# Kernel optimization log

Hardware: AMD Instinct MI355X
Metric: run time of the kernel (lower is better)

The kernel has to match this reference:

```python
import jax, jax.numpy as jnp
import numpy as np


def _make_area_table():
    # Surrogate for create_table_neighbour_code_to_surface_area((1,1,1)):
    # a fixed 256-entry lookup that is exactly 0 for the all-empty (0) and
    # all-full (255) neighbour codes and strictly positive otherwise, which
    # preserves the structure the loss relies on (gt_surface = area > 0,
    # gt_foreground = code==255, gt_background = code==0).
    pop = np.array([bin(c).count("1") for c in range(256)], dtype=np.float32)
    return (0.5 * np.minimum(pop, 8.0 - pop)).astype(np.float32)


def _conv3d(x, w):
    # x: [B,1,D,H,W], w: [1,1,2,2,2], VALID 2x2x2 sliding window
    return jax.lax.conv_general_dilated(
        x, w, window_strides=(1, 1, 1), padding="VALID",
        dimension_numbers=("NCDHW", "OIDHW", "NCDHW"))


def setup_inputs() -> dict:
    key = jax.random.key(0)
    k1, k2 = jax.random.split(key)
    B, D, H, W = 2, 128, 256, 256
    preds = jax.random.normal(k1, (B, 1, D, H, W), dtype=jnp.float32)
    targets = jax.random.randint(k2, (B, 1, D, H, W), 0, 2).astype(jnp.float32)
    power = (2.0 ** jnp.arange(8, dtype=jnp.float32)).reshape(1, 1, 2, 2, 2)
    kernel = jnp.ones((1, 1, 2, 2, 2), dtype=jnp.float32)
    area = jnp.asarray(_make_area_table())
    return {"preds": preds, "targets": targets, "power": power,
            "kernel": kernel, "area": area}


def reference(preds, targets, power, kernel, area):
    eps = 1e-5
    bsz = preds.shape[0]

    # log-prob that all 8 voxels of each 2x2x2 cube are foreground / background
    fg = jnp.exp(_conv3d(jax.nn.log_sigmoid(preds), kernel)).reshape(bsz, -1)
    bg = jnp.exp(_conv3d(jax.nn.log_sigmoid(-preds), kernel)).reshape(bsz, -1)
    surf = 1.0 - fg - bg

    # neighbour codes from binary targets (no grad path)
    codes = jax.lax.stop_gradient(_conv3d(targets, power)).astype(jnp.int32).reshape(bsz, -1)
    gt_area = area[codes.reshape(-1)].reshape(bsz, -1)
    gt_fg = (codes == 255).astype(jnp.float32)
    gt_bg = (codes == 0).astype(jnp.float32)
    gt_surf = (gt_area > 0).astype(jnp.float32)

    fg_dice = (2.0 * jnp.sum(fg * gt_fg, -1) + eps) / (jnp.sum(fg, -1) + jnp.sum(gt_fg, -1) + eps)
    bg_dice = (2.0 * jnp.sum(bg * gt_bg, -1) + eps) / (jnp.sum(bg, -1) + jnp.sum(gt_bg, -1) + eps)
    surf_dice = (2.0 * jnp.sum(surf * gt_area, -1) + eps) / (jnp.sum((surf + gt_surf) * gt_area, -1) + eps)

    dice = (fg_dice + bg_dice + surf_dice) / 3.0
    return 1.0 - jnp.mean(dice)
```

## Files before the change

### kernel.cpp

```cpp
#include <hip/hip_runtime.h>

typedef float f2 __attribute__((ext_vector_type(2)));

#define DD 128
#define HH 256
#define WW 256
#define OD 127
#define SLICE_F (HH*WW)
#define NBIN 64
#define CHUNK 8
#define ROWS_B 9216
#define STAGE_B 18432
#define NBUF 2

#define VMCNT0() asm volatile("s_waitcnt vmcnt(0)" ::: "memory")

struct Sl { f2 uu2[4]; f2 vv2[4]; f2 ps[4]; };

__device__ __forceinline__ void stage_slice(const float* __restrict__ pB,
                                            const float* __restrict__ tB,
                                            int slice, char* lb,
                                            int h0, int wv, int lane)
{
    #pragma unroll
    for (int i = 0; i < 5; ++i) {
        if (i == 4 && wv >= 2) break;
        const int L = i * 4 + wv;
        const int T = (L >= 9) ? 1 : 0;
        const int r = L - T * 9;
        const int grow = min(h0 + r, HH - 1);
        const float* g = (T ? tB : pB)
                       + ((size_t)slice << 16) + (grow << 8) + (lane << 2);
        void* l = lb + T * ROWS_B + r * 1024 + lane * 16;
        __builtin_amdgcn_global_load_lds(
            (const __attribute__((address_space(1))) void*)g,
            (__attribute__((address_space(3))) void*)l, 16, 0, 0);
    }
}

__device__ __forceinline__ void make_sl_lds(const char* buf, int wv, int lane, Sl& S)
{
    const float* sp = (const float*)buf;
    const float* st = (const float*)(buf + ROWS_B);
    const int ro = ((wv << 1) << 8) + (lane << 2);
    const float4 p0 = *(const float4*)(sp + ro);
    const float4 p1 = *(const float4*)(sp + ro + 256);
    const float4 p2 = *(const float4*)(sp + ro + 512);
    const float4 t0 = *(const float4*)(st + ro);
    const float4 t1 = *(const float4*)(st + ro + 256);
    const float4 t2 = *(const float4*)(st + ro + 512);

    float u0x=__expf(p0.x), u0y=__expf(p0.y), u0z=__expf(p0.z), u0w=__expf(p0.w);
    float u1x=__expf(p1.x), u1y=__expf(p1.y), u1z=__expf(p1.z), u1w=__expf(p1.w);
    float u2x=__expf(p2.x), u2y=__expf(p2.y), u2z=__expf(p2.z), u2w=__expf(p2.w);

    f2 uA0 = {u0x,u1x}, uB0 = {u1x,u2x};
    f2 uA1 = {u0y,u1y}, uB1 = {u1y,u2y};
    f2 uA2 = {u0z,u1z}, uB2 = {u1z,u2z};
    f2 uA3 = {u0w,u1w}, uB3 = {u1w,u2w};

    f2 W0 = uA0*uB0, W1 = uA1*uB1, W2 = uA2*uB2, W3 = uA3*uB3;
    f2 Q0 = (uA0+1.f)*(uB0+1.f);
    f2 Q1 = (uA1+1.f)*(uB1+1.f);
    f2 Q2 = (uA2+1.f)*(uB2+1.f);
    f2 Q3 = (uA3+1.f)*(uB3+1.f);
    f2 W4, Q4;
    W4.x = __shfl_down(W0.x, 1); W4.y = __shfl_down(W0.y, 1);
    Q4.x = __shfl_down(Q0.x, 1); Q4.y = __shfl_down(Q0.y, 1);

    S.uu2[0]=W0*W1; S.uu2[1]=W1*W2; S.uu2[2]=W2*W3; S.uu2[3]=W3*W4;
    S.vv2[0]=Q0*Q1; S.vv2[1]=Q1*Q2; S.vv2[2]=Q2*Q3; S.vv2[3]=Q3*Q4;

    f2 cs0 = {t0.x+t1.x, t1.x+t2.x};
    f2 cs1 = {t0.y+t1.y, t1.y+t2.y};
    f2 cs2 = {t0.z+t1.z, t1.z+t2.z};
    f2 cs3 = {t0.w+t1.w, t1.w+t2.w};
    f2 cs4; cs4.x = __shfl_down(cs0.x, 1); cs4.y = __shfl_down(cs0.y, 1);
    S.ps[0]=cs0+cs1; S.ps[1]=cs1+cs2; S.ps[2]=cs2+cs3; S.ps[3]=cs3+cs4;
}

__device__ __forceinline__ void do_cubes(const Sl& P, const Sl& C,
        const f2 vAll, const f2 v3,
        f2& aFG, f2& aF255, f2& aBG, f2& aBG0, f2& aSFA,
        f2& c255, f2& c0, f2& cMN)
{
    #pragma unroll
    for (int j = 0; j < 4; ++j) {
        f2 E = P.uu2[j] * C.uu2[j];
        f2 Q = P.vv2[j] * C.vv2[j];
        f2 vj = (j == 3) ? v3 : vAll;
        f2 r; r.x = __builtin_amdgcn_rcpf(Q.x); r.y = __builtin_amdgcn_rcpf(Q.y);
        r *= vj;
        f2 fg = E * r;
        f2 pop = P.ps[j] + C.ps[j];
        f2 i255, i0, mn;
        i255.x = fmaxf(pop.x - 7.f, 0.f); i255.y = fmaxf(pop.y - 7.f, 0.f);
        i0.x   = fmaxf(1.f - pop.x, 0.f); i0.y   = fmaxf(1.f - pop.y, 0.f);
        mn.x   = 4.f - fabsf(pop.x - 4.f); mn.y = 4.f - fabsf(pop.y - 4.f);
        mn *= vj;
        aFG  += fg;
        aBG  += r;
        aF255 = fg * i255 + aF255;
        aBG0  = r  * i0   + aBG0;
        c255  = i255 * vj + c255;
        c0    = i0   * vj + c0;
        aSFA  = (fg + r) * mn + aSFA;
        cMN  += mn;
    }
}

#define LAYER(SRC, DST, STAGE_OFF, READ_OFF)                                   \
    do {                                                                       \
        VMCNT0();                                                              \
        __builtin_amdgcn_s_barrier();                                          \
        __builtin_amdgcn_sched_barrier(0);                                     \
        if (t + 2 <= NT)                                                       \
            stage_slice(pB, tB, d0 + t + 2, smem + (STAGE_OFF), h0, wv, lane); \
        make_sl_lds(smem + (READ_OFF), wv, lane, DST);                         \
        do_cubes(SRC, DST, vAll, v3, aFG, aF255, aBG, aBG0, aSFA, c255, c0, cMN); \
    } while (0)

__global__ __launch_bounds__(256, 4)
void loss_main(const float* __restrict__ preds,
               const float* __restrict__ targets,
               float* __restrict__ ws)
{
    __shared__ __align__(16) char smem[NBUF * STAGE_B];

    const int lane = threadIdx.x & 63;
    const int wv   = threadIdx.x >> 6;

    const int nid = ((blockIdx.x & 7) << 7) + (blockIdx.x >> 3);
    const int x = nid & 31;
    const int y = (nid >> 5) & 15;
    const int b = nid >> 9;

    const int h0 = x << 3;
    const int d0 = y << 3;
    const int NT = min(CHUNK, OD - d0);

    const float* pB = preds   + (size_t)b * DD * SLICE_F;
    const float* tB = targets + (size_t)b * DD * SLICE_F;

    const int   myrow = h0 + (wv << 1);
    const float rv1 = (myrow + 1 < HH - 1) ? 1.f : 0.f;
    const float v63 = (lane == 63) ? 0.f : 1.f;
    const f2 vAll = {1.f, rv1};
    const f2 v3   = {v63, v63 * rv1};

    f2 aFG={0,0}, aF255={0,0}, aBG={0,0}, aBG0={0,0}, aSFA={0,0};
    f2 c255={0,0}, c0={0,0}, cMN={0,0};

    stage_slice(pB, tB, d0,     smem,           h0, wv, lane);
    stage_slice(pB, tB, d0 + 1, smem + STAGE_B, h0, wv, lane);
    VMCNT0();
    __builtin_amdgcn_s_barrier();
    __builtin_amdgcn_sched_barrier(0);

    Sl A, B;
    make_sl_lds(smem, wv, lane, A);

    int t = 0;
    for (;;) {
        LAYER(A, B, 0, STAGE_B);
        if (++t >= NT) break;
        LAYER(B, A, STAGE_B, 0);
        if (++t >= NT) break;
    }

    float acc[8] = {aFG.x+aFG.y, aF255.x+aF255.y, c255.x+c255.y,
                    aBG.x+aBG.y, aBG0.x+aBG0.y,   c0.x+c0.y,
                    aSFA.x+aSFA.y, cMN.x+cMN.y};
    #pragma unroll
    for (int i = 0; i < 8; ++i) {
        float v = acc[i];
        #pragma unroll
        for (int off = 32; off > 0; off >>= 1) v += __shfl_xor(v, off);
        acc[i] = v;
    }
    float mine = acc[0];
    mine = (lane == 1) ? acc[1] : mine;
    mine = (lane == 2) ? acc[2] : mine;
    mine = (lane == 3) ? acc[3] : mine;
    mine = (lane == 4) ? acc[4] : mine;
    mine = (lane == 5) ? acc[5] : mine;
    mine = (lane == 6) ? acc[6] : mine;
    mine = (lane == 7) ? acc[7] : mine;
    if (lane < 8) {
        int bin = nid & (NBIN - 1);
        atomicAdd(&ws[(bin * 2 + b) * 8 + lane], mine);
    }
}

__global__ void loss_final(const float* __restrict__ ws, float* __restrict__ out)
{
    __shared__ float s[16];
    const int t = threadIdx.x;
    if (t < 16) {
        float v = 0.f;
        #pragma unroll 4
        for (int x = 0; x < NBIN; ++x) v += ws[x * 16 + t];
        s[t] = v;
    }
    __syncthreads();
    if (t == 0) {
        const float eps = 1e-5f;
        float dice = 0.f;
        #pragma unroll
        for (int b = 0; b < 2; ++b) {
            const float* q = s + b * 8;
            float fg_dice = (2.f*q[1] + eps) / (q[0] + q[2] + eps);
            float bg_dice = (2.f*q[4] + eps) / (q[3] + q[5] + eps);
            float q6 = 0.5f * q[6];
            float q7 = 0.5f * q[7];
            float ss = q7 - q6;
            float sf_dice = (2.f*ss + eps) / (ss + q7 + eps);
            dice += fg_dice + bg_dice + sf_dice;
        }
        out[0] = 1.f - dice * (1.f/6.f);
    }
}

extern "C" void kernel_launch(void* const* d_in, const int* in_sizes, int n_in,
                              void* d_out, int out_size, void* d_ws, size_t ws_size,
                              hipStream_t stream)
{
    const float* preds   = (const float*)d_in[0];
    const float* targets = (const float*)d_in[1];
    float* ws = (float*)d_ws;

    hipMemsetAsync(ws, 0, NBIN * 16 * sizeof(float), stream);

    loss_main<<<1024, 256, 0, stream>>>(preds, targets, ws);
    loss_final<<<1, 64, 0, stream>>>(ws, (float*)d_out);
}
```

Baseline: 40.77 us.

## Pack binary targets into bitmasks in a pre-pass and halve depth chunk

Adds a pre-pass kernel that packs the float targets into 1-bit masks (bit 29 of the float encoding separates 0.0 from 1.0). The main kernel then stages these compact bits into LDS and builds the neighbour-code popcounts with __popc, instead of staging and summing full float target rows. The depth chunk per block is halved, the grid doubled, and the launch-bounds occupancy hint raised from 4 to 8, since the smaller LDS footprint allows more resident blocks. In exchange it adds an extra kernel launch and a full read of targets in the pre-pass, and halving the chunk raises how often slices are reloaded at chunk boundaries.

```diff
diff --git a/kernel.cpp b/kernel.cpp
--- a/kernel.cpp
+++ b/kernel.cpp
@@ -8,47 +8,71 @@
 #define OD 127
 #define SLICE_F (HH*WW)
 #define NBIN 64
-#define CHUNK 8
-#define ROWS_B 9216
-#define STAGE_B 18432
+#define CHUNK 4
+#define PRED_B 9216
+#define BITS_B 512
+#define STAGE_B (PRED_B + BITS_B)
 #define NBUF 2
+#define WS_BITS_OFF 4096
 
 #define VMCNT0() asm volatile("s_waitcnt vmcnt(0)" ::: "memory")
 
 struct Sl { f2 uu2[4]; f2 vv2[4]; f2 ps[4]; };
 
+__global__ __launch_bounds__(256)
+void pack_bits(const float* __restrict__ t, unsigned int* __restrict__ bits)
+{
+    const int tid = blockIdx.x * 256 + threadIdx.x;
+    const float4* p = (const float4*)(t + ((size_t)tid << 5));
+    unsigned int acc = 0;
+    #pragma unroll
+    for (int i = 0; i < 8; ++i) {
+        float4 v = p[i];
+        unsigned int n = ((__float_as_uint(v.x) >> 29) & 1u)
+                       | (((__float_as_uint(v.y) >> 29) & 1u) << 1)
+                       | (((__float_as_uint(v.z) >> 29) & 1u) << 2)
+                       | (((__float_as_uint(v.w) >> 29) & 1u) << 3);
+        acc |= n << (i * 4);
+    }
+    bits[tid] = acc;
+}
+
 __device__ __forceinline__ void stage_slice(const float* __restrict__ pB,
-                                            const float* __restrict__ tB,
+                                            const unsigned int* __restrict__ bB,
                                             int slice, char* lb,
                                             int h0, int wv, int lane)
 {
     #pragma unroll
-    for (int i = 0; i < 5; ++i) {
-        if (i == 4 && wv >= 2) break;
-        const int L = i * 4 + wv;
-        const int T = (L >= 9) ? 1 : 0;
-        const int r = L - T * 9;
-        const int grow = min(h0 + r, HH - 1);
-        const float* g = (T ? tB : pB)
-                       + ((size_t)slice << 16) + (grow << 8) + (lane << 2);
-        void* l = lb + T * ROWS_B + r * 1024 + lane * 16;
-        __builtin_amdgcn_global_load_lds(
-            (const __attribute__((address_space(1))) void*)g,
-            (__attribute__((address_space(3))) void*)l, 16, 0, 0);
+    for (int i = 0; i < 3; ++i) {
+        const int slot = i * 4 + wv;
+        if (slot < 9) {
+            const int grow = min(h0 + slot, HH - 1);
+            const float* g = pB + ((size_t)slice << 16) + (grow << 8) + (lane << 2);
+            void* l = lb + slot * 1024 + lane * 16;
+            __builtin_amdgcn_global_load_lds(
+                (const __attribute__((address_space(1))) void*)g,
+                (__attribute__((address_space(3))) void*)l, 16, 0, 0);
+        } else if (slot < 11) {
+            const int half = slot - 9;
+            const int row  = (half << 3) + (lane >> 3);
+            const int grow = min(h0 + row, HH - 1);
+            const unsigned int* g = bB + (((size_t)slice * HH + grow) << 3) + (lane & 7);
+            void* l = lb + PRED_B + half * 256 + lane * 4;
+            __builtin_amdgcn_global_load_lds(
+                (const __attribute__((address_space(1))) void*)g,
+                (__attribute__((address_space(3))) void*)l, 4, 0, 0);
+        }
     }
 }
 
 __device__ __forceinline__ void make_sl_lds(const char* buf, int wv, int lane, Sl& S)
 {
     const float* sp = (const float*)buf;
-    const float* st = (const float*)(buf + ROWS_B);
+    const unsigned int* bl = (const unsigned int*)(buf + PRED_B);
     const int ro = ((wv << 1) << 8) + (lane << 2);
     const float4 p0 = *(const float4*)(sp + ro);
     const float4 p1 = *(const float4*)(sp + ro + 256);
     const float4 p2 = *(const float4*)(sp + ro + 512);
-    const float4 t0 = *(const float4*)(st + ro);
-    const float4 t1 = *(const float4*)(st + ro + 256);
-    const float4 t2 = *(const float4*)(st + ro + 512);
 
     float u0x=__expf(p0.x), u0y=__expf(p0.y), u0z=__expf(p0.z), u0w=__expf(p0.w);
     float u1x=__expf(p1.x), u1y=__expf(p1.y), u1z=__expf(p1.z), u1w=__expf(p1.w);
@@ -71,12 +95,22 @@
     S.uu2[0]=W0*W1; S.uu2[1]=W1*W2; S.uu2[2]=W2*W3; S.uu2[3]=W3*W4;
     S.vv2[0]=Q0*Q1; S.vv2[1]=Q1*Q2; S.vv2[2]=Q2*Q3; S.vv2[3]=Q3*Q4;
 
-    f2 cs0 = {t0.x+t1.x, t1.x+t2.x};
-    f2 cs1 = {t0.y+t1.y, t1.y+t2.y};
-    f2 cs2 = {t0.z+t1.z, t1.z+t2.z};
-    f2 cs3 = {t0.w+t1.w, t1.w+t2.w};
-    f2 cs4; cs4.x = __shfl_down(cs0.x, 1); cs4.y = __shfl_down(cs0.y, 1);
-    S.ps[0]=cs0+cs1; S.ps[1]=cs1+cs2; S.ps[2]=cs2+cs3; S.ps[3]=cs3+cs4;
+    const int r = wv << 1;
+    const int q = lane >> 3;
+    const int sh = (lane & 7) << 2;
+    unsigned int a0 = bl[r*8 + q],     a1 = bl[r*8 + q + 1];
+    unsigned int b0 = bl[(r+1)*8 + q], b1 = bl[(r+1)*8 + q + 1];
+    unsigned int c0 = bl[(r+2)*8 + q], c1 = bl[(r+2)*8 + q + 1];
+    unsigned int m0 = (unsigned int)(((((unsigned long long)a1) << 32) | a0) >> sh) & 0x1Fu;
+    unsigned int m1 = (unsigned int)(((((unsigned long long)b1) << 32) | b0) >> sh) & 0x1Fu;
+    unsigned int m2 = (unsigned int)(((((unsigned long long)c1) << 32) | c0) >> sh) & 0x1Fu;
+    unsigned int M01 = m0 | (m1 << 8);
+    unsigned int M12 = m1 | (m2 << 8);
+    #pragma unroll
+    for (int j = 0; j < 4; ++j) {
+        S.ps[j].x = (float)__popc((M01 >> j) & 0x303u);
+        S.ps[j].y = (float)__popc((M12 >> j) & 0x303u);
+    }
 }
 
 __device__ __forceinline__ void do_cubes(const Sl& P, const Sl& C,
@@ -115,14 +149,14 @@
         __builtin_amdgcn_s_barrier();                                          \
         __builtin_amdgcn_sched_barrier(0);                                     \
         if (t + 2 <= NT)                                                       \
-            stage_slice(pB, tB, d0 + t + 2, smem + (STAGE_OFF), h0, wv, lane); \
+            stage_slice(pB, bB, d0 + t + 2, smem + (STAGE_OFF), h0, wv, lane); \
         make_sl_lds(smem + (READ_OFF), wv, lane, DST);                         \
         do_cubes(SRC, DST, vAll, v3, aFG, aF255, aBG, aBG0, aSFA, c255, c0, cMN); \
     } while (0)
 
-__global__ __launch_bounds__(256, 4)
+__global__ __launch_bounds__(256, 8)
 void loss_main(const float* __restrict__ preds,
-               const float* __restrict__ targets,
+               const unsigned int* __restrict__ bits,
                float* __restrict__ ws)
 {
     __shared__ __align__(16) char smem[NBUF * STAGE_B];
@@ -130,17 +164,17 @@
     const int lane = threadIdx.x & 63;
     const int wv   = threadIdx.x >> 6;
 
-    const int nid = ((blockIdx.x & 7) << 7) + (blockIdx.x >> 3);
+    const int nid = ((blockIdx.x & 7) << 8) + (blockIdx.x >> 3);
     const int x = nid & 31;
-    const int y = (nid >> 5) & 15;
-    const int b = nid >> 9;
+    const int y = (nid >> 5) & 31;
+    const int b = nid >> 10;
 
     const int h0 = x << 3;
-    const int d0 = y << 3;
+    const int d0 = y << 2;
     const int NT = min(CHUNK, OD - d0);
 
-    const float* pB = preds   + (size_t)b * DD * SLICE_F;
-    const float* tB = targets + (size_t)b * DD * SLICE_F;
+    const float*        pB = preds + (size_t)b * DD * SLICE_F;
+    const unsigned int* bB = bits  + (size_t)b * DD * HH * 8;
 
     const int   myrow = h0 + (wv << 1);
     const float rv1 = (myrow + 1 < HH - 1) ? 1.f : 0.f;
@@ -151,8 +185,8 @@
     f2 aFG={0,0}, aF255={0,0}, aBG={0,0}, aBG0={0,0}, aSFA={0,0};
     f2 c255={0,0}, c0={0,0}, cMN={0,0};
 
-    stage_slice(pB, tB, d0,     smem,           h0, wv, lane);
-    stage_slice(pB, tB, d0 + 1, smem + STAGE_B, h0, wv, lane);
+    stage_slice(pB, bB, d0,     smem,           h0, wv, lane);
+    stage_slice(pB, bB, d0 + 1, smem + STAGE_B, h0, wv, lane);
     VMCNT0();
     __builtin_amdgcn_s_barrier();
     __builtin_amdgcn_sched_barrier(0);
@@ -228,9 +262,11 @@
     const float* preds   = (const float*)d_in[0];
     const float* targets = (const float*)d_in[1];
     float* ws = (float*)d_ws;
+    unsigned int* bitsbuf = (unsigned int*)((char*)d_ws + WS_BITS_OFF);
 
     hipMemsetAsync(ws, 0, NBIN * 16 * sizeof(float), stream);
 
-    loss_main<<<1024, 256, 0, stream>>>(preds, targets, ws);
+    pack_bits<<<2048, 256, 0, stream>>>(targets, bitsbuf);
+    loss_main<<<2048, 256, 0, stream>>>(preds, bitsbuf, ws);
     loss_final<<<1, 64, 0, stream>>>(ws, (float*)d_out);
 }
```

Measured after the change: 162.0 us. 297% more time.

## Triple-buffer preds in LDS, load targets to registers, drop memset and atomics

Applied to the files above, without the earlier changes.

Preds rows are now staged through a three-slot LDS ring using async global-to-LDS loads, while target rows and the halo pred row are loaded straight into registers one layer ahead. Waits use partial vmcnt counts instead of draining everything, so more loads stay in flight across the barrier. The final reduction now writes per-block partials to the workspace without atomics, which removes the memset launch; loss_final gains more threads to sum the 1024 partials. The cost is more registers, tricky vmcnt accounting that depends on load ordering, and redundant global loads of overlapping target rows.

```diff
diff --git a/kernel.cpp b/kernel.cpp
--- a/kernel.cpp
+++ b/kernel.cpp
@@ -7,48 +7,60 @@
 #define WW 256
 #define OD 127
 #define SLICE_F (HH*WW)
-#define NBIN 64
 #define CHUNK 8
-#define ROWS_B 9216
-#define STAGE_B 18432
-#define NBUF 2
+#define ROW_B 1024
+#define SLOT_B 8192
+#define NBUF 3
 
 #define VMCNT0() asm volatile("s_waitcnt vmcnt(0)" ::: "memory")
+#define WAITP() do { if (wv == 3) asm volatile("s_waitcnt vmcnt(6)" ::: "memory"); \
+                     else         asm volatile("s_waitcnt vmcnt(5)" ::: "memory"); } while (0)
 
 struct Sl { f2 uu2[4]; f2 vv2[4]; f2 ps[4]; };
 
-__device__ __forceinline__ void stage_slice(const float* __restrict__ pB,
-                                            const float* __restrict__ tB,
-                                            int slice, char* lb,
+__device__ __forceinline__ void stage_slice(const float* __restrict__ pB, int s,
+                                            char* smem, int slot,
                                             int h0, int wv, int lane)
 {
     #pragma unroll
-    for (int i = 0; i < 5; ++i) {
-        if (i == 4 && wv >= 2) break;
-        const int L = i * 4 + wv;
-        const int T = (L >= 9) ? 1 : 0;
-        const int r = L - T * 9;
-        const int grow = min(h0 + r, HH - 1);
-        const float* g = (T ? tB : pB)
-                       + ((size_t)slice << 16) + (grow << 8) + (lane << 2);
-        void* l = lb + T * ROWS_B + r * 1024 + lane * 16;
+    for (int i = 0; i < 2; ++i) {
+        const int row = (wv << 1) + i;
+        const float* g = pB + ((size_t)s << 16) + ((size_t)(h0 + row) << 8) + (lane << 2);
+        void* l = smem + slot * SLOT_B + row * ROW_B + lane * 16;
         __builtin_amdgcn_global_load_lds(
             (const __attribute__((address_space(1))) void*)g,
             (__attribute__((address_space(3))) void*)l, 16, 0, 0);
     }
 }
 
-__device__ __forceinline__ void make_sl_lds(const char* buf, int wv, int lane, Sl& S)
+__device__ __forceinline__ void load_tregs(const float* __restrict__ tB,
+                                           const float* __restrict__ pB, int s,
+                                           int h0, int wv, int lane,
+                                           float4& t0, float4& t1, float4& t2, float4& p8)
+{
+    const int r0 = h0 + (wv << 1);
+    const size_t base = ((size_t)s << 16) + (lane << 2);
+    t0 = *(const float4*)(tB + base + ((size_t)r0 << 8));
+    t1 = *(const float4*)(tB + base + ((size_t)(r0 + 1) << 8));
+    const int r2 = min(r0 + 2, HH - 1);
+    t2 = *(const float4*)(tB + base + ((size_t)r2 << 8));
+    if (wv == 3) {
+        const int r8 = min(h0 + 8, HH - 1);
+        p8 = *(const float4*)(pB + base + ((size_t)r8 << 8));
+    }
+}
+
+__device__ __forceinline__ void make_sl(const char* buf, int wv, int lane,
+                                        float4 t0, float4 t1, float4 t2, float4 p8,
+                                        Sl& S)
 {
     const float* sp = (const float*)buf;
-    const float* st = (const float*)(buf + ROWS_B);
     const int ro = ((wv << 1) << 8) + (lane << 2);
     const float4 p0 = *(const float4*)(sp + ro);
     const float4 p1 = *(const float4*)(sp + ro + 256);
-    const float4 p2 = *(const float4*)(sp + ro + 512);
-    const float4 t0 = *(const float4*)(st + ro);
-    const float4 t1 = *(const float4*)(st + ro + 256);
-    const float4 t2 = *(const float4*)(st + ro + 512);
+    float4 p2;
+    if (wv < 3) p2 = *(const float4*)(sp + ro + 512);
+    else        p2 = p8;
 
     float u0x=__expf(p0.x), u0y=__expf(p0.y), u0z=__expf(p0.z), u0w=__expf(p0.w);
     float u1x=__expf(p1.x), u1y=__expf(p1.y), u1z=__expf(p1.z), u1w=__expf(p1.w);
@@ -109,15 +121,21 @@
     }
 }
 
-#define LAYER(SRC, DST, STAGE_OFF, READ_OFF)                                   \
+#define LAYER(SRC, DST, Ut0, Ut1, Ut2, Up8, It0, It1, It2, Ip8)                \
     do {                                                                       \
-        VMCNT0();                                                              \
+        if (t + 2 <= NT) {                                                     \
+            load_tregs(tB, pB, d0 + t + 2, h0, wv, lane, It0, It1, It2, Ip8);  \
+            WAITP();                                                           \
+        } else {                                                               \
+            VMCNT0();                                                          \
+        }                                                                      \
         __builtin_amdgcn_s_barrier();                                          \
+        if (t + 3 <= NT) stage_slice(pB, d0 + t + 3, smem, sw, h0, wv, lane);  \
         __builtin_amdgcn_sched_barrier(0);                                     \
-        if (t + 2 <= NT)                                                       \
-            stage_slice(pB, tB, d0 + t + 2, smem + (STAGE_OFF), h0, wv, lane); \
-        make_sl_lds(smem + (READ_OFF), wv, lane, DST);                         \
+        make_sl(smem + sr * SLOT_B, wv, lane, Ut0, Ut1, Ut2, Up8, DST);        \
         do_cubes(SRC, DST, vAll, v3, aFG, aF255, aBG, aBG0, aSFA, c255, c0, cMN); \
+        if (++sr == NBUF) sr = 0;                                              \
+        if (++sw == NBUF) sw = 0;                                              \
     } while (0)
 
 __global__ __launch_bounds__(256, 4)
@@ -125,7 +143,8 @@
                const float* __restrict__ targets,
                float* __restrict__ ws)
 {
-    __shared__ __align__(16) char smem[NBUF * STAGE_B];
+    __shared__ __align__(16) char smem[NBUF * SLOT_B];
+    __shared__ float red[32];
 
     const int lane = threadIdx.x & 63;
     const int wv   = threadIdx.x >> 6;
@@ -151,20 +170,27 @@
     f2 aFG={0,0}, aF255={0,0}, aBG={0,0}, aBG0={0,0}, aSFA={0,0};
     f2 c255={0,0}, c0={0,0}, cMN={0,0};
 
-    stage_slice(pB, tB, d0,     smem,           h0, wv, lane);
-    stage_slice(pB, tB, d0 + 1, smem + STAGE_B, h0, wv, lane);
-    VMCNT0();
+    float4 u0={0,0,0,0}, u1=u0, u2=u0, up8=u0;
+    float4 v0=u0, v1=u0, v2=u0, vp8=u0;
+
+    load_tregs(tB, pB, d0,     h0, wv, lane, u0, u1, u2, up8);
+    stage_slice(pB, d0,     smem, 0, h0, wv, lane);
+    stage_slice(pB, d0 + 1, smem, 1, h0, wv, lane);
+    load_tregs(tB, pB, d0 + 1, h0, wv, lane, v0, v1, v2, vp8);
+    WAITP();
     __builtin_amdgcn_s_barrier();
+    stage_slice(pB, d0 + 2, smem, 2, h0, wv, lane);
     __builtin_amdgcn_sched_barrier(0);
 
     Sl A, B;
-    make_sl_lds(smem, wv, lane, A);
-
+    make_sl(smem, wv, lane, u0, u1, u2, up8, A);
+
+    int sr = 1, sw = 0;
     int t = 0;
     for (;;) {
-        LAYER(A, B, 0, STAGE_B);
+        LAYER(A, B, v0, v1, v2, vp8, u0, u1, u2, up8);
         if (++t >= NT) break;
-        LAYER(B, A, STAGE_B, 0);
+        LAYER(B, A, u0, u1, u2, up8, v0, v1, v2, vp8);
         if (++t >= NT) break;
     }
 
@@ -186,29 +212,40 @@
     mine = (lane == 5) ? acc[5] : mine;
     mine = (lane == 6) ? acc[6] : mine;
     mine = (lane == 7) ? acc[7] : mine;
-    if (lane < 8) {
-        int bin = nid & (NBIN - 1);
-        atomicAdd(&ws[(bin * 2 + b) * 8 + lane], mine);
-    }
+    if (lane < 8) red[wv * 8 + lane] = mine;
+    __syncthreads();
+    if (wv == 0 && lane < 8)
+        ws[nid * 8 + lane] = red[lane] + red[8 + lane] + red[16 + lane] + red[24 + lane];
 }
 
 __global__ void loss_final(const float* __restrict__ ws, float* __restrict__ out)
 {
-    __shared__ float s[16];
-    const int t = threadIdx.x;
-    if (t < 16) {
-        float v = 0.f;
-        #pragma unroll 4
-        for (int x = 0; x < NBIN; ++x) v += ws[x * 16 + t];
-        s[t] = v;
-    }
+    __shared__ float part[16][17];
+    __shared__ float S[16];
+    const int tid = threadIdx.x;
+    const int c = tid >> 4, sub = tid & 15;
+    const int bb = c >> 3, s = c & 7;
+    float v = 0.f;
+    #pragma unroll 4
+    for (int k = 0; k < 32; ++k) {
+        int nid = bb * 512 + sub * 32 + k;
+        v += ws[nid * 8 + s];
+    }
+    part[c][sub] = v;
     __syncthreads();
-    if (t == 0) {
+    if (tid < 16) {
+        float q = 0.f;
+        #pragma unroll
+        for (int i = 0; i < 16; ++i) q += part[tid][i];
+        S[tid] = q;
+    }
+    __syncthreads();
+    if (tid == 0) {
         const float eps = 1e-5f;
         float dice = 0.f;
         #pragma unroll
-        for (int b = 0; b < 2; ++b) {
-            const float* q = s + b * 8;
+        for (int b2 = 0; b2 < 2; ++b2) {
+            const float* q = S + b2 * 8;
             float fg_dice = (2.f*q[1] + eps) / (q[0] + q[2] + eps);
             float bg_dice = (2.f*q[4] + eps) / (q[3] + q[5] + eps);
             float q6 = 0.5f * q[6];
@@ -229,8 +266,6 @@
     const float* targets = (const float*)d_in[1];
     float* ws = (float*)d_ws;
 
-    hipMemsetAsync(ws, 0, NBIN * 16 * sizeof(float), stream);
-
     loss_main<<<1024, 256, 0, stream>>>(preds, targets, ws);
-    loss_final<<<1, 64, 0, stream>>>(ws, (float*)d_out);
-}
+    loss_final<<<1, 256, 0, stream>>>(ws, (float*)d_out);
+}
```

After: 47.52 us. +16.6%, slower.
